# Kernel optimization log

Measured on AMD Instinct MI355X. Metric: run time of the kernel, lower is better.

The kernel has to match this reference:

```python
import math
import jax, jax.numpy as jnp
import numpy as np

B, S, C = 2048, 64, 142
D, H, DH, FF, L = 256, 8, 32, 512, 3
E, K = 128, 1024
EPS = 1e-5

def _ln(x, g, b):
    m = jnp.mean(x, -1, keepdims=True)
    v = jnp.var(x, -1, keepdims=True)
    return (x - m) * jax.lax.rsqrt(v + EPS) * g + b

def _pe(seq_len, d):
    pos = jnp.arange(seq_len, dtype=jnp.float32)[:, None]
    div = jnp.exp(jnp.arange(0, d, 2, dtype=jnp.float32) * (-math.log(10000.0) / d))
    pe = jnp.zeros((seq_len, d), jnp.float32)
    pe = pe.at[:, 0::2].set(jnp.sin(pos * div))
    pe = pe.at[:, 1::2].set(jnp.cos(pos * div))
    return pe

def setup_inputs() -> dict:
    key = jax.random.key(0)
    ks = iter(jax.random.split(key, 40))
    r = lambda shape, s=0.02: jax.random.normal(next(ks), shape, jnp.float32) * s
    inp = {
        'x': jax.random.normal(next(ks), (B, S, C), jnp.float32),
        'W_in': r((D, C)), 'b_in': jnp.zeros((D,), jnp.float32),
        'cls_token': jax.random.normal(next(ks), (1, 1, D), jnp.float32),
        'Wqkv': r((L, 3 * D, D)), 'bqkv': jnp.zeros((L, 3 * D), jnp.float32),
        'Wo': r((L, D, D)), 'bo': jnp.zeros((L, D), jnp.float32),
        'W1': r((L, FF, D)), 'b1': jnp.zeros((L, FF), jnp.float32),
        'W2': r((L, D, FF)), 'b2': jnp.zeros((L, D), jnp.float32),
        'ln1_g': jnp.ones((L, D), jnp.float32), 'ln1_b': jnp.zeros((L, D), jnp.float32),
        'ln2_g': jnp.ones((L, D), jnp.float32), 'ln2_b': jnp.zeros((L, D), jnp.float32),
        'lnf_g': jnp.ones((D,), jnp.float32), 'lnf_b': jnp.zeros((D,), jnp.float32),
        'W_out': r((E, D)), 'b_out': jnp.zeros((E,), jnp.float32),
        'codebook': jax.random.normal(next(ks), (K, E), jnp.float32),
        'Wd1': r((D, E)), 'bd1': jnp.zeros((D,), jnp.float32),
        'lnd_g': jnp.ones((D,), jnp.float32), 'lnd_b': jnp.zeros((D,), jnp.float32),
        'Wd2': r((128, D)), 'bd2': jnp.zeros((128,), jnp.float32),
        'Wd3': r((2, 128)), 'bd3': jnp.zeros((2,), jnp.float32),
    }
    return inp

def _forward(x, W_in, b_in, cls_token, Wqkv, bqkv, Wo, bo, W1, b1, W2, b2,
             ln1_g, ln1_b, ln2_g, ln2_b, lnf_g, lnf_b, W_out, b_out, codebook,
             Wd1, bd1, lnd_g, lnd_b, Wd2, bd2, Wd3, bd3):
    b = x.shape[0]
    h = x @ W_in.T + b_in                      # [B,S,D]
    h = h + _pe(S, D)[None]
    h = jnp.concatenate([jnp.broadcast_to(cls_token, (b, 1, D)), h], axis=1)  # [B,T,D]
    T = S + 1
    for i in range(L):
        qkv = h @ Wqkv[i].T + bqkv[i]          # [B,T,3D]
        q, k, v = jnp.split(qkv, 3, axis=-1)
        q = q.reshape(b, T, H, DH).transpose(0, 2, 1, 3)
        k = k.reshape(b, T, H, DH).transpose(0, 2, 1, 3)
        v = v.reshape(b, T, H, DH).transpose(0, 2, 1, 3)
        scores = jnp.einsum('bhqd,bhkd->bhqk', q, k) / math.sqrt(DH)
        attn = jax.nn.softmax(scores, axis=-1)
        o = jnp.einsum('bhqk,bhkd->bhqd', attn, v).transpose(0, 2, 1, 3).reshape(b, T, D)
        h = _ln(h + (o @ Wo[i].T + bo[i]), ln1_g[i], ln1_b[i])
        ff = jax.nn.gelu(h @ W1[i].T + b1[i], approximate=False) @ W2[i].T + b2[i]
        h = _ln(h + ff, ln2_g[i], ln2_b[i])
    cls_out = h[:, 0, :]
    z_e = _ln(cls_out, lnf_g, lnf_b) @ W_out.T + b_out   # [B,E]
    # --- EMA VQ (eval): squared-dist argmin + codebook gather ---
    d2 = (jnp.sum(z_e * z_e, -1, keepdims=True)
          - 2.0 * (z_e @ codebook.T)
          + jnp.sum(codebook * codebook, -1)[None, :])   # [B,K]
    indices = jnp.argmin(d2, axis=-1)                    # [B]
    z_q = codebook[indices]                              # gather [B,E]
    commitment_loss = 0.1 * jnp.mean((jax.lax.stop_gradient(z_q) - z_e) ** 2)
    z_q_st = z_e + jax.lax.stop_gradient(z_q - z_e)      # straight-through
    avg_probs = jnp.zeros((K,), jnp.float32).at[indices].add(1.0) / b
    perplexity = jnp.exp(-jnp.sum(avg_probs * jnp.log(avg_probs + 1e-10)))
    # --- decoder ---
    d = jax.nn.gelu(_ln(z_q_st @ Wd1.T + bd1, lnd_g, lnd_b), approximate=False)
    d = jax.nn.gelu(d @ Wd2.T + bd2, approximate=False)
    velocity_pred = d @ Wd3.T + bd3                      # [B,2]
    return velocity_pred, indices, commitment_loss, perplexity

def reference(x, W_in, b_in, cls_token, Wqkv, bqkv, Wo, bo, W1, b1, W2, b2,
              ln1_g, ln1_b, ln2_g, ln2_b, lnf_g, lnf_b, W_out, b_out, codebook,
              Wd1, bd1, lnd_g, lnd_b, Wd2, bd2, Wd3, bd3):
    return _forward(x, W_in, b_in, cls_token, Wqkv, bqkv, Wo, bo, W1, b1, W2, b2,
                    ln1_g, ln1_b, ln2_g, ln2_b, lnf_g, lnf_b, W_out, b_out, codebook,
                    Wd1, bd1, lnd_g, lnd_b, Wd2, bd2, Wd3, bd3)
```

## Files before the change

kernel.cpp:

```cpp
#include <hip/hip_runtime.h>
#include <math.h>

#define NB   2048
#define SEQ  64
#define CIN  142
#define DM   256
#define NH   8
#define DHD  32
#define FFD  512
#define NL   3
#define ED   128
#define KCB  1024
#define TT   65
#define NT   512

#define E_TOT    1572864
#define OFF_WO   589824
#define OFF_W1   786432
#define OFF_W2   1179648
#define WS_NEED  (4224 + 4 * E_TOT)

typedef __attribute__((ext_vector_type(4))) float f32x4;
typedef __attribute__((ext_vector_type(8))) _Float16 f16x8;
typedef __attribute__((ext_vector_type(4))) _Float16 f16x4;
typedef __attribute__((ext_vector_type(2))) _Float16 f16x2;

#define LO_SCALE 2048.0f
#define LO_INV   (1.0f / 2048.0f)

__device__ __forceinline__ float gelu_f(float x) {
  return 0.5f * x * (1.0f + erff(x * 0.70710678118654752f));
}

__device__ __forceinline__ float wave_bsum(float v) {
#pragma unroll
  for (int off = 32; off >= 1; off >>= 1) v += __shfl_xor(v, off, 64);
  return v;
}
__device__ __forceinline__ float wave_bmax(float v) {
#pragma unroll
  for (int off = 32; off >= 1; off >>= 1) v = fmaxf(v, __shfl_xor(v, off, 64));
  return v;
}

__device__ __forceinline__ int pidx(int pitch, int t, int c) {
  return t * pitch + ((((c >> 3) ^ (t & 7)) << 3) | (c & 7));
}

__device__ __forceinline__ void split4v(f32x4 v, f16x4& hi, f16x4& lo) {
#pragma unroll
  for (int j = 0; j < 4; ++j) {
    _Float16 h = (_Float16)v[j];
    hi[j] = h;
    lo[j] = (_Float16)((v[j] - (float)h) * LO_SCALE);
  }
}

__device__ __forceinline__ void pair_store4(_Float16* dH, _Float16* dL, int pitch,
                                            int t, int o, f32x4 v) {
  f16x4 hi, lo;
  split4v(v, hi, lo);
  int off = pidx(pitch, t, o);
  *(f16x4*)&dH[off] = hi;
  *(f16x4*)&dL[off] = lo;
}
__device__ __forceinline__ f32x4 pair_load4(const _Float16* dH, const _Float16* dL,
                                            int pitch, int t, int o) {
  int off = pidx(pitch, t, o);
  f16x4 hi = *(const f16x4*)&dH[off];
  f16x4 lo = *(const f16x4*)&dL[off];
  f32x4 v;
#pragma unroll
  for (int j = 0; j < 4; ++j) v[j] = (float)hi[j] + (float)lo[j] * LO_INV;
  return v;
}

__device__ __forceinline__ void split8_arr(const float* vv, f16x8& hi, f16x8& lo) {
#pragma unroll
  for (int j = 0; j < 8; ++j) {
    _Float16 h = (_Float16)vv[j];
    hi[j] = h;
    lo[j] = (_Float16)((vv[j] - (float)h) * LO_SCALE);
  }
}
__device__ __forceinline__ void split8_f4(const float* p, f16x8& hi, f16x8& lo) {
  float4 v0 = *(const float4*)p;
  float4 v1 = *(const float4*)(p + 4);
  float vv[8] = {v0.x, v0.y, v0.z, v0.w, v1.x, v1.y, v1.z, v1.w};
  split8_arr(vv, hi, lo);
}
__device__ __forceinline__ void split8_f2(const float* p, f16x8& hi, f16x8& lo) {
  float vv[8];
#pragma unroll
  for (int j = 0; j < 4; ++j) {
    float2 v = *(const float2*)(p + 2 * j);
    vv[2 * j] = v.x;
    vv[2 * j + 1] = v.y;
  }
  split8_arr(vv, hi, lo);
}

template <int TTN, int CIT, bool GUARDO, int WMODE>
__device__ __forceinline__ void mfma_gemm2(
    f32x4 (&acc1)[CIT][TTN], f32x4 (&acc2)[CIT][TTN],
    const float* __restrict__ Wg, const _Float16* __restrict__ WgH,
    const _Float16* __restrict__ WgL, int wld, int rbase, int rsel, int otiles,
    const _Float16* aH, const _Float16* aL, int apitch, int tRows,
    int kdim, int kvalid, int wave, int lane) {
  const int q4 = lane >> 4, cl = lane & 15;
  if (GUARDO && wave >= otiles) return;
  int wrow[CIT];
  bool oval[CIT];
#pragma unroll
  for (int ci = 0; ci < CIT; ++ci) {
    int ot = wave + 8 * ci;
    oval[ci] = !GUARDO || (ot < otiles);
    int r = ot * 16 + cl;
    int grow = rbase + (r & 31) + rsel * (r >> 5);
    wrow[ci] = grow * wld;
  }
  f16x8 zf;
#pragma unroll
  for (int j = 0; j < 8; ++j) zf[j] = (_Float16)0.f;
#pragma unroll 1
  for (int kc = 0; kc < kdim; kc += 32) {
    f16x8 bh[CIT], bl[CIT];
#pragma unroll
    for (int ci = 0; ci < CIT; ++ci) {
      if (oval[ci]) {
        if (WMODE == 2) {
          int off = wrow[ci] + kc + 8 * q4;
          bh[ci] = *(const f16x8*)&WgH[off];
          bl[ci] = *(const f16x8*)&WgL[off];
        } else if (WMODE == 1) {
          split8_f4(Wg + wrow[ci] + kc + 8 * q4, bh[ci], bl[ci]);
        } else {
          const float* wp = Wg + wrow[ci] + kc + 8 * q4;
          int cb = kc + 8 * q4;
          float vv[8];
#pragma unroll
          for (int j = 0; j < 8; ++j) vv[j] = (cb + j < kvalid) ? wp[j] : 0.f;
          split8_arr(vv, bh[ci], bl[ci]);
        }
      } else {
        bh[ci] = zf;
        bl[ci] = zf;
      }
    }
#pragma unroll
    for (int tt = 0; tt < TTN; ++tt) {
      int t = 16 * tt + cl;
      f16x8 ah, al;
      if (t < tRows) {
        int off = t * apitch + (((((kc >> 3) + q4) ^ (t & 7))) << 3);
        ah = *(const f16x8*)&aH[off];
        al = *(const f16x8*)&aL[off];
      } else {
        ah = zf;
        al = zf;
      }
#pragma unroll
      for (int ci = 0; ci < CIT; ++ci) {
        if (oval[ci]) {
          acc1[ci][tt] = __builtin_amdgcn_mfma_f32_16x16x32_f16(bh[ci], ah, acc1[ci][tt], 0, 0, 0);
          acc2[ci][tt] = __builtin_amdgcn_mfma_f32_16x16x32_f16(bh[ci], al, acc2[ci][tt], 0, 0, 0);
          acc2[ci][tt] = __builtin_amdgcn_mfma_f32_16x16x32_f16(bl[ci], ah, acc2[ci][tt], 0, 0, 0);
        }
      }
    }
  }
}

__device__ __forceinline__ void qkv_epi(const f32x4* a1, const f32x4* a2, int nt,
                                        int base, int tvalid,
                                        const float* __restrict__ bqkv_l, int hd,
                                        float* Qf, float* Kf, float* VT, float* ex,
                                        int wave, int lane) {
  if (wave >= 6) return;
  const int q4 = lane >> 4, cl = lane & 15;
  for (int tt = 0; tt < nt; ++tt) {
    int tl = 16 * tt + cl;
    if (tl < tvalid) {
      int t = base + tl;
#pragma unroll
      for (int rg = 0; rg < 4; ++rg) {
        int c = wave * 16 + q4 * 4 + rg;
        int d = c & 31;
        float v = a1[tt][rg] + a2[tt][rg] * LO_INV +
                  bqkv_l[(c >> 5) * 256 + hd * 32 + d];
        if (c < 32)      { if (t < 64) Qf[t * 36 + d] = v; else ex[d] = v; }
        else if (c < 64) { if (t < 64) Kf[t * 36 + d] = v; else ex[32 + d] = v; }
        else             VT[d * 66 + t] = v;
      }
    }
  }
}

__device__ __forceinline__ void proj_epi(const f32x4* a1, const f32x4* a2, int nt,
                                         int base, int tvalid, int half,
                                         const float* __restrict__ bo_l,
                                         _Float16* hH, _Float16* hL,
                                         int wave, int lane) {
  const int q4 = lane >> 4, cl = lane & 15;
  for (int tt = 0; tt < nt; ++tt) {
    int tl = 16 * tt + cl;
    if (tl < tvalid) {
      int t = base + tl;
      int o = half * 128 + wave * 16 + q4 * 4;
      f32x4 r = pair_load4(hH, hL, 256, t, o);
      float4 b4 = *(const float4*)&bo_l[o];
      float bb[4] = {b4.x, b4.y, b4.z, b4.w};
      f32x4 v;
#pragma unroll
      for (int rg = 0; rg < 4; ++rg)
        v[rg] = r[rg] + a1[tt][rg] + a2[tt][rg] * LO_INV + bb[rg];
      pair_store4(hH, hL, 256, t, o, v);
    }
  }
}

__device__ __forceinline__ void ln_rows_pair(_Float16* hH, _Float16* hL,
                                             const float* g, const float* be,
                                             int wave, int lane) {
  for (int t = wave; t < TT; t += 8) {
    int c0 = 2 * lane, c1 = 128 + 2 * lane;
    int o0 = pidx(256, t, c0), o1 = pidx(256, t, c1);
    f16x2 h0 = *(f16x2*)&hH[o0], l0 = *(f16x2*)&hL[o0];
    f16x2 h1 = *(f16x2*)&hH[o1], l1 = *(f16x2*)&hL[o1];
    float v0 = (float)h0[0] + (float)l0[0] * LO_INV;
    float v1 = (float)h0[1] + (float)l0[1] * LO_INV;
    float v2 = (float)h1[0] + (float)l1[0] * LO_INV;
    float v3 = (float)h1[1] + (float)l1[1] * LO_INV;
    float m = wave_bsum(v0 + v1 + v2 + v3) * (1.0f / 256.0f);
    float d0 = v0 - m, d1 = v1 - m, d2 = v2 - m, d3 = v3 - m;
    float var = wave_bsum(d0 * d0 + d1 * d1 + d2 * d2 + d3 * d3) * (1.0f / 256.0f);
    float rstd = 1.0f / sqrtf(var + 1e-5f);
    float2 g0 = *(const float2*)&g[c0], g1 = *(const float2*)&g[c1];
    float2 b0 = *(const float2*)&be[c0], b1 = *(const float2*)&be[c1];
    float r0 = d0 * rstd * g0.x + b0.x;
    float r1 = d1 * rstd * g0.y + b0.y;
    float r2 = d2 * rstd * g1.x + b1.x;
    float r3 = d3 * rstd * g1.y + b1.y;
    f16x2 nh0, nl0, nh1, nl1;
    nh0[0] = (_Float16)r0; nl0[0] = (_Float16)((r0 - (float)nh0[0]) * LO_SCALE);
    nh0[1] = (_Float16)r1; nl0[1] = (_Float16)((r1 - (float)nh0[1]) * LO_SCALE);
    nh1[0] = (_Float16)r2; nl1[0] = (_Float16)((r2 - (float)nh1[0]) * LO_SCALE);
    nh1[1] = (_Float16)r3; nl1[1] = (_Float16)((r3 - (float)nh1[1]) * LO_SCALE);
    *(f16x2*)&hH[o0] = nh0; *(f16x2*)&hL[o0] = nl0;
    *(f16x2*)&hH[o1] = nh1; *(f16x2*)&hL[o1] = nl1;
  }
}

template <int WM>
__device__ __forceinline__ void ff_pass0(const float* __restrict__ W1_l,
                                         const float* __restrict__ b1_l,
                                         const float* __restrict__ W2_l,
                                         const float* __restrict__ b2_l,
                                         const _Float16* __restrict__ W1H,
                                         const _Float16* __restrict__ W1L,
                                         const _Float16* __restrict__ W2H,
                                         const _Float16* __restrict__ W2L,
                                         _Float16* hH, _Float16* hL,
                                         _Float16* f1H, _Float16* f1L,
                                         int wave, int lane) {
  const int q4 = lane >> 4, cl = lane & 15;
  const f32x4 Z4 = {0.f, 0.f, 0.f, 0.f};
  for (int half = 0; half < 2; ++half) {
    f32x4 a1[2][2], a2[2][2];
#pragma unroll
    for (int ci = 0; ci < 2; ++ci)
#pragma unroll
      for (int tt = 0; tt < 2; ++tt) { a1[ci][tt] = Z4; a2[ci][tt] = Z4; }
    mfma_gemm2<2, 2, false, WM>(a1, a2, W1_l, W1H, W1L, DM, half * 256, 32, 16,
                                hH, hL, 256, 32, DM, DM, wave, lane);
#pragma unroll
    for (int ci = 0; ci < 2; ++ci)
#pragma unroll
      for (int tt = 0; tt < 2; ++tt) {
        int t = 16 * tt + cl;
        int m = half * 256 + (wave + 8 * ci) * 16 + q4 * 4;
        float4 b4 = *(const float4*)&b1_l[m];
        float bb[4] = {b4.x, b4.y, b4.z, b4.w};
        f32x4 v;
#pragma unroll
        for (int rg = 0; rg < 4; ++rg)
          v[rg] = gelu_f(a1[ci][tt][rg] + a2[ci][tt][rg] * LO_INV + bb[rg]);
        pair_store4(f1H, f1L, 512, t, m, v);
      }
  }
  __syncthreads();
  {
    f32x4 a1[2][2], a2[2][2];
#pragma unroll
    for (int ci = 0; ci < 2; ++ci)
#pragma unroll
      for (int tt = 0; tt < 2; ++tt) { a1[ci][tt] = Z4; a2[ci][tt] = Z4; }
    mfma_gemm2<2, 2, false, WM>(a1, a2, W2_l, W2H, W2L, FFD, 0, 32, 16,
                                f1H, f1L, 512, 32, FFD, FFD, wave, lane);
#pragma unroll
    for (int ci = 0; ci < 2; ++ci)
#pragma unroll
      for (int tt = 0; tt < 2; ++tt) {
        int t = 16 * tt + cl;
        int o = (wave + 8 * ci) * 16 + q4 * 4;
        f32x4 r = pair_load4(hH, hL, 256, t, o);
        float4 b4 = *(const float4*)&b2_l[o];
        float bb[4] = {b4.x, b4.y, b4.z, b4.w};
        f32x4 v;
#pragma unroll
        for (int rg = 0; rg < 4; ++rg)
          v[rg] = r[rg] + a1[ci][tt][rg] + a2[ci][tt][rg] * LO_INV + bb[rg];
        pair_store4(hH, hL, 256, t, o, v);
      }
  }
}

template <int WM>
__device__ __forceinline__ void ff_pass1(const float* __restrict__ W1_l,
                                         const float* __restrict__ b1_l,
                                         const float* __restrict__ W2_l,
                                         const float* __restrict__ b2_l,
                                         const _Float16* __restrict__ W1H,
                                         const _Float16* __restrict__ W1L,
                                         const _Float16* __restrict__ W2H,
                                         const _Float16* __restrict__ W2L,
                                         _Float16* hH, _Float16* hL,
                                         _Float16* f1H, _Float16* f1L,
                                         int wave, int lane) {
  const int q4 = lane >> 4, cl = lane & 15;
  const f32x4 Z4 = {0.f, 0.f, 0.f, 0.f};
  for (int cg = 0; cg < 4; ++cg) {
    f32x4 a1[1][3], a2[1][3];
#pragma unroll
    for (int tt = 0; tt < 3; ++tt) { a1[0][tt] = Z4; a2[0][tt] = Z4; }
    mfma_gemm2<3, 1, false, WM>(a1, a2, W1_l, W1H, W1L, DM, cg * 128, 32, 8,
                                hH + 32 * 256, hL + 32 * 256, 256, 33, DM, DM,
                                wave, lane);
#pragma unroll
    for (int tt = 0; tt < 3; ++tt) {
      int tl = 16 * tt + cl;
      if (tl < 33) {
        int m = cg * 128 + wave * 16 + q4 * 4;
        float4 b4 = *(const float4*)&b1_l[m];
        float bb[4] = {b4.x, b4.y, b4.z, b4.w};
        f32x4 v;
#pragma unroll
        for (int rg = 0; rg < 4; ++rg)
          v[rg] = gelu_f(a1[0][tt][rg] + a2[0][tt][rg] * LO_INV + bb[rg]);
        pair_store4(f1H, f1L, 512, tl, m, v);
      }
    }
  }
  __syncthreads();
  for (int cg = 0; cg < 2; ++cg) {
    f32x4 a1[1][3], a2[1][3];
#pragma unroll
    for (int tt = 0; tt < 3; ++tt) { a1[0][tt] = Z4; a2[0][tt] = Z4; }
    mfma_gemm2<3, 1, false, WM>(a1, a2, W2_l, W2H, W2L, FFD, cg * 128, 32, 8,
                                f1H, f1L, 512, 33, FFD, FFD, wave, lane);
#pragma unroll
    for (int tt = 0; tt < 3; ++tt) {
      int tl = 16 * tt + cl;
      if (tl < 33) {
        int t = 32 + tl;
        int o = cg * 128 + wave * 16 + q4 * 4;
        f32x4 r = pair_load4(hH, hL, 256, t, o);
        float4 b4 = *(const float4*)&b2_l[o];
        float bb[4] = {b4.x, b4.y, b4.z, b4.w};
        f32x4 v;
#pragma unroll
        for (int rg = 0; rg < 4; ++rg)
          v[rg] = r[rg] + a1[0][tt][rg] + a2[0][tt][rg] * LO_INV + bb[rg];
        pair_store4(hH, hL, 256, t, o, v);
      }
    }
  }
}

__global__ void vqvae_zero(float* __restrict__ ws) {
  int i = blockIdx.x * blockDim.x + threadIdx.x;
  if (i < 1025) ws[i] = 0.f;
}

__global__ void vqvae_prep(const float* __restrict__ Wqkv,
                           const float* __restrict__ Wo,
                           const float* __restrict__ W1,
                           const float* __restrict__ W2,
                           float* __restrict__ ws) {
  _Float16* PH = (_Float16*)(ws + 1056);
  _Float16* PL = PH + E_TOT;
  for (int i = blockIdx.x * blockDim.x + threadIdx.x; i < E_TOT;
       i += gridDim.x * blockDim.x) {
    float v;
    if (i < OFF_WO)      v = Wqkv[i];
    else if (i < OFF_W1) v = Wo[i - OFF_WO];
    else if (i < OFF_W2) v = W1[i - OFF_W1];
    else                 v = W2[i - OFF_W2];
    _Float16 h = (_Float16)v;
    PH[i] = h;
    PL[i] = (_Float16)((v - (float)h) * LO_SCALE);
  }
}

__global__ __attribute__((amdgpu_flat_work_group_size(512, 512), amdgpu_waves_per_eu(2, 2)))
void vqvae_main(
    const float* __restrict__ x, const float* __restrict__ W_in,
    const float* __restrict__ b_in, const float* __restrict__ cls_token,
    const float* __restrict__ Wqkv, const float* __restrict__ bqkv,
    const float* __restrict__ Wo, const float* __restrict__ bo,
    const float* __restrict__ W1, const float* __restrict__ b1,
    const float* __restrict__ W2, const float* __restrict__ b2,
    const float* __restrict__ ln1_g, const float* __restrict__ ln1_b,
    const float* __restrict__ ln2_g, const float* __restrict__ ln2_b,
    const float* __restrict__ lnf_g, const float* __restrict__ lnf_b,
    const float* __restrict__ W_out, const float* __restrict__ b_out,
    const float* __restrict__ codebook, const float* __restrict__ Wd1,
    const float* __restrict__ bd1, const float* __restrict__ lnd_g,
    const float* __restrict__ lnd_b, const float* __restrict__ Wd2,
    const float* __restrict__ bd2, const float* __restrict__ Wd3,
    const float* __restrict__ bd3, float* __restrict__ out,
    float* __restrict__ ws, int usePre) {
  __shared__ __align__(16) float hbuf[16640];
  __shared__ __align__(16) float obuf[16896];
  __shared__ __align__(16) float scr[6768];

  const int tid = threadIdx.x;
  const int b = blockIdx.x;
  const int lane = tid & 63, wave = tid >> 6;
  const int q4 = lane >> 4, cl = lane & 15;
  const f32x4 Z4 = {0.f, 0.f, 0.f, 0.f};
  _Float16* hH = (_Float16*)hbuf;
  _Float16* hL = hH + 65 * 256;
  const _Float16* WH = (const _Float16*)(ws + 1056);
  const _Float16* WL = WH + E_TOT;

  {
    _Float16* xH = (_Float16*)obuf;
    _Float16* xL = xH + 64 * 256;
    for (int f = tid; f < SEQ * 160; f += NT) {
      int r = f / 160, c = f - r * 160;
      float v = (c < CIN) ? x[(size_t)b * (SEQ * CIN) + r * CIN + c] : 0.f;
      _Float16 h = (_Float16)v;
      int off = pidx(256, r, c);
      xH[off] = h;
      xL[off] = (_Float16)((v - (float)h) * LO_SCALE);
    }
    if (tid < DM) {
      float v = cls_token[tid];
      _Float16 h = (_Float16)v;
      hH[tid] = h;
      hL[tid] = (_Float16)((v - (float)h) * LO_SCALE);
    }
    __syncthreads();
    for (int half = 0; half < 2; ++half) {
      for (int tg = 0; tg < 2; ++tg) {
        f32x4 a1[1][2], a2[1][2];
#pragma unroll
        for (int tt = 0; tt < 2; ++tt) { a1[0][tt] = Z4; a2[0][tt] = Z4; }
        mfma_gemm2<2, 1, false, 0>(a1, a2, W_in, nullptr, nullptr, CIN,
                                   half * 128, 32, 8, xH + 32 * tg * 256,
                                   xL + 32 * tg * 256, 256, 32, 160, CIN,
                                   wave, lane);
#pragma unroll
        for (int tt = 0; tt < 2; ++tt) {
          int t = 32 * tg + 16 * tt + cl;
          int o = half * 128 + wave * 16 + q4 * 4;
          f32x4 v;
#pragma unroll
          for (int rg = 0; rg < 4; ++rg) {
            int d = o + rg;
            float div = expf(-(float)(d & ~1) * (9.210340371976184f / 256.0f));
            float ang = (float)t * div;
            float pe = (d & 1) ? cosf(ang) : sinf(ang);
            v[rg] = a1[0][tt][rg] + a2[0][tt][rg] * LO_INV + b_in[d] + pe;
          }
          pair_store4(hH, hL, 256, t + 1, o, v);
        }
      }
    }
  }
  __syncthreads();

  for (int li = 0; li < NL; ++li) {
    const float* Wqkv_l = Wqkv + (size_t)li * 768 * DM;
    const float* bqkv_l = bqkv + li * 768;
    const float* Wo_l = Wo + (size_t)li * DM * DM;
    const float* bo_l = bo + li * DM;
    const float* W1_l = W1 + (size_t)li * FFD * DM;
    const float* b1_l = b1 + li * FFD;
    const float* W2_l = W2 + (size_t)li * DM * FFD;
    const float* b2_l = b2 + li * DM;
    const _Float16* WqkvH_l = WH + (size_t)li * 768 * DM;
    const _Float16* WqkvL_l = WL + (size_t)li * 768 * DM;
    const _Float16* WoH_l = WH + OFF_WO + (size_t)li * DM * DM;
    const _Float16* WoL_l = WL + OFF_WO + (size_t)li * DM * DM;
    const _Float16* W1H_l = WH + OFF_W1 + (size_t)li * FFD * DM;
    const _Float16* W1L_l = WL + OFF_W1 + (size_t)li * FFD * DM;
    const _Float16* W2H_l = WH + OFF_W2 + (size_t)li * DM * FFD;
    const _Float16* W2L_l = WL + OFF_W2 + (size_t)li * DM * FFD;
    _Float16* oH = (_Float16*)obuf;
    _Float16* oL = oH + 65 * 256;
    float* ex = obuf + 16640;

    for (int hd = 0; hd < NH; ++hd) {
      float* Qf = scr;
      float* Kf = scr + 2304;
      float* VT = scr + 4608;
      float* Sb = scr;
      {
        f32x4 a1[1][3], a2[1][3];
#pragma unroll
        for (int tt = 0; tt < 3; ++tt) { a1[0][tt] = Z4; a2[0][tt] = Z4; }
        if (usePre)
          mfma_gemm2<3, 1, true, 2>(a1, a2, nullptr, WqkvH_l, WqkvL_l, DM,
                                    hd * 32, 256, 6, hH, hL, 256, 48, DM, DM,
                                    wave, lane);
        else
          mfma_gemm2<3, 1, true, 1>(a1, a2, Wqkv_l, nullptr, nullptr, DM,
                                    hd * 32, 256, 6, hH, hL, 256, 48, DM, DM,
                                    wave, lane);
        __syncthreads();
        qkv_epi(&a1[0][0], &a2[0][0], 3, 0, 48, bqkv_l, hd, Qf, Kf, VT, ex,
                wave, lane);
        f32x4 c1[1][2], c2[1][2];
#pragma unroll
        for (int tt = 0; tt < 2; ++tt) { c1[0][tt] = Z4; c2[0][tt] = Z4; }
        if (usePre)
          mfma_gemm2<2, 1, true, 2>(c1, c2, nullptr, WqkvH_l, WqkvL_l, DM,
                                    hd * 32, 256, 6, hH + 48 * 256,
                                    hL + 48 * 256, 256, 17, DM, DM, wave, lane);
        else
          mfma_gemm2<2, 1, true, 1>(c1, c2, Wqkv_l, nullptr, nullptr, DM,
                                    hd * 32, 256, 6, hH + 48 * 256,
                                    hL + 48 * 256, 256, 17, DM, DM, wave, lane);
        qkv_epi(&c1[0][0], &c2[0][0], 2, 48, 17, bqkv_l, hd, Qf, Kf, VT, ex,
                wave, lane);
      }
      __syncthreads();
      f32x4 s1[4], s2[4];
      if (wave < 4) {
#pragma unroll
        for (int i = 0; i < 4; ++i) { s1[i] = Z4; s2[i] = Z4; }
        f16x8 bh, bl;
        split8_f4(&Kf[(16 * wave + cl) * 36 + 8 * q4], bh, bl);
#pragma unroll
        for (int rt = 0; rt < 4; ++rt) {
          f16x8 ah, al;
          split8_f4(&Qf[(16 * rt + cl) * 36 + 8 * q4], ah, al);
          s1[rt] = __builtin_amdgcn_mfma_f32_16x16x32_f16(ah, bh, s1[rt], 0, 0, 0);
          s2[rt] = __builtin_amdgcn_mfma_f32_16x16x32_f16(ah, bl, s2[rt], 0, 0, 0);
          s2[rt] = __builtin_amdgcn_mfma_f32_16x16x32_f16(al, bh, s2[rt], 0, 0, 0);
        }
      } else {
        const int tt4 = wave - 4;
        {
          float vv[8];
#pragma unroll
          for (int j = 0; j < 8; ++j) {
            float v = ex[32 + 8 * q4 + j];
            vv[j] = (cl == 0) ? v : 0.f;
          }
          f16x8 kh, kl;
          split8_arr(vv, kh, kl);
          f16x8 qh, ql;
          split8_f4(&Qf[(16 * tt4 + cl) * 36 + 8 * q4], qh, ql);
          f32x4 c1 = Z4, c2 = Z4;
          c1 = __builtin_amdgcn_mfma_f32_16x16x32_f16(qh, kh, c1, 0, 0, 0);
          c2 = __builtin_amdgcn_mfma_f32_16x16x32_f16(qh, kl, c2, 0, 0, 0);
          c2 = __builtin_amdgcn_mfma_f32_16x16x32_f16(ql, kh, c2, 0, 0, 0);
          if (cl == 0) {
#pragma unroll
            for (int rg = 0; rg < 4; ++rg)
              ex[64 + 16 * tt4 + q4 * 4 + rg] = c1[rg] + c2[rg] * LO_INV;
          }
        }
        {
          float vv[8];
#pragma unroll
          for (int j = 0; j < 8; ++j) {
            float v = ex[8 * q4 + j];
            vv[j] = (cl == 0) ? v : 0.f;
          }
          f16x8 qh, ql;
          split8_arr(vv, qh, ql);
          f16x8 kh, kl;
          split8_f4(&Kf[(16 * tt4 + cl) * 36 + 8 * q4], kh, kl);
          f32x4 r1 = Z4, r2 = Z4;
          r1 = __builtin_amdgcn_mfma_f32_16x16x32_f16(qh, kh, r1, 0, 0, 0);
          r2 = __builtin_amdgcn_mfma_f32_16x16x32_f16(qh, kl, r2, 0, 0, 0);
          r2 = __builtin_amdgcn_mfma_f32_16x16x32_f16(ql, kh, r2, 0, 0, 0);
          if (q4 == 0) ex[128 + 16 * tt4 + cl] = r1[0] + r2[0] * LO_INV;
        }
        if (wave == 4) {
          float p = ex[lane & 31] * ex[32 + (lane & 31)];
          p = wave_bsum(p) * 0.5f;
          if (lane == 0) ex[128 + 64] = p;
        }
      }
      __syncthreads();
      if (wave < 4) {
#pragma unroll
        for (int rt = 0; rt < 4; ++rt)
#pragma unroll
          for (int rg = 0; rg < 4; ++rg)
            Sb[(rt * 16 + q4 * 4 + rg) * 66 + wave * 16 + cl] =
                s1[rt][rg] + s2[rt][rg] * LO_INV;
      } else if (wave == 4) {
        Sb[lane * 66 + 64] = ex[64 + lane];
      } else if (wave == 5) {
        Sb[64 * 66 + lane] = ex[128 + lane];
        if (lane == 0) Sb[64 * 66 + 64] = ex[128 + 64];
      }
      __syncthreads();
      {
        const float sc = 0.17677669529663687f;
        for (int t = wave; t < 65; t += 8) {
          float s = Sb[t * 66 + lane] * sc;
          float s64 = Sb[t * 66 + 64] * sc;
          float m = fmaxf(wave_bmax(s), s64);
          float e = __expf(s - m), e64 = __expf(s64 - m);
          float inv = 1.0f / (wave_bsum(e) + e64);
          Sb[t * 66 + lane] = e * inv;
          if (lane == 0) Sb[t * 66 + 64] = e64 * inv;
        }
      }
      __syncthreads();
      {
        int rt = wave >> 1, ct = wave & 1;
        f32x4 o1 = Z4, o2 = Z4;
#pragma unroll
        for (int kc = 0; kc < 64; kc += 32) {
          f16x8 ph, pl, vh, vl;
          split8_f2(&Sb[(16 * rt + cl) * 66 + kc + 8 * q4], ph, pl);
          split8_f2(&VT[(16 * ct + cl) * 66 + kc + 8 * q4], vh, vl);
          o1 = __builtin_amdgcn_mfma_f32_16x16x32_f16(vh, ph, o1, 0, 0, 0);
          o2 = __builtin_amdgcn_mfma_f32_16x16x32_f16(vh, pl, o2, 0, 0, 0);
          o2 = __builtin_amdgcn_mfma_f32_16x16x32_f16(vl, ph, o2, 0, 0, 0);
        }
        int t = rt * 16 + cl;
        float p64 = Sb[t * 66 + 64];
        int ob = ct * 16 + q4 * 4;
        f32x4 v;
#pragma unroll
        for (int rg = 0; rg < 4; ++rg) {
          int d = ob + rg;
          v[rg] = o1[rg] + o2[rg] * LO_INV + p64 * VT[d * 66 + 64];
        }
        pair_store4(oH, oL, 256, t, hd * 32 + ob, v);
      }
      if (wave == 0) {
        int d = lane & 31, hf = lane >> 5;
        float o = 0.f;
        for (int u = hf * 32; u < hf * 32 + 32; ++u)
          o += Sb[64 * 66 + u] * VT[d * 66 + u];
        if (hf == 1) o += Sb[64 * 66 + 64] * VT[d * 66 + 64];
        o += __shfl_down(o, 32, 64);
        if (lane < 32) {
          int c = hd * 32 + d;
          _Float16 h = (_Float16)o;
          int off = pidx(256, 64, c);
          oH[off] = h;
          oL[off] = (_Float16)((o - (float)h) * LO_SCALE);
        }
      }
    }
    __syncthreads();

    for (int half = 0; half < 2; ++half) {
      {
        f32x4 a1[1][3], a2[1][3];
#pragma unroll
        for (int tt = 0; tt < 3; ++tt) { a1[0][tt] = Z4; a2[0][tt] = Z4; }
        if (usePre)
          mfma_gemm2<3, 1, false, 2>(a1, a2, nullptr, WoH_l, WoL_l, DM,
                                     half * 128, 32, 8, oH, oL, 256, 48, DM,
                                     DM, wave, lane);
        else
          mfma_gemm2<3, 1, false, 1>(a1, a2, Wo_l, nullptr, nullptr, DM,
                                     half * 128, 32, 8, oH, oL, 256, 48, DM,
                                     DM, wave, lane);
        proj_epi(&a1[0][0], &a2[0][0], 3, 0, 48, half, bo_l, hH, hL, wave, lane);
      }
      {
        f32x4 a1[1][2], a2[1][2];
#pragma unroll
        for (int tt = 0; tt < 2; ++tt) { a1[0][tt] = Z4; a2[0][tt] = Z4; }
        if (usePre)
          mfma_gemm2<2, 1, false, 2>(a1, a2, nullptr, WoH_l, WoL_l, DM,
                                     half * 128, 32, 8, oH + 48 * 256,
                                     oL + 48 * 256, 256, 17, DM, DM, wave, lane);
        else
          mfma_gemm2<2, 1, false, 1>(a1, a2, Wo_l, nullptr, nullptr, DM,
                                     half * 128, 32, 8, oH + 48 * 256,
                                     oL + 48 * 256, 256, 17, DM, DM, wave, lane);
        proj_epi(&a1[0][0], &a2[0][0], 2, 48, 17, half, bo_l, hH, hL, wave, lane);
      }
    }
    __syncthreads();
    ln_rows_pair(hH, hL, ln1_g + li * DM, ln1_b + li * DM, wave, lane);
    __syncthreads();

    {
      _Float16* f1H = (_Float16*)obuf;
      _Float16* f1L = f1H + 33 * 512;
      if (usePre) {
        ff_pass0<2>(W1_l, b1_l, W2_l, b2_l, W1H_l, W1L_l, W2H_l, W2L_l,
                    hH, hL, f1H, f1L, wave, lane);
        __syncthreads();
        ff_pass1<2>(W1_l, b1_l, W2_l, b2_l, W1H_l, W1L_l, W2H_l, W2L_l,
                    hH, hL, f1H, f1L, wave, lane);
      } else {
        ff_pass0<1>(W1_l, b1_l, W2_l, b2_l, nullptr, nullptr, nullptr, nullptr,
                    hH, hL, f1H, f1L, wave, lane);
        __syncthreads();
        ff_pass1<1>(W1_l, b1_l, W2_l, b2_l, nullptr, nullptr, nullptr, nullptr,
                    hH, hL, f1H, f1L, wave, lane);
      }
    }
    __syncthreads();
    ln_rows_pair(hH, hL, ln2_g + li * DM, ln2_b + li * DM, wave, lane);
    __syncthreads();
  }

  if (tid < 64) {
    int c0 = 2 * lane, c1 = 128 + 2 * lane;
    float v0 = (float)hH[c0] + (float)hL[c0] * LO_INV;
    float v1 = (float)hH[c0 + 1] + (float)hL[c0 + 1] * LO_INV;
    float v2 = (float)hH[c1] + (float)hL[c1] * LO_INV;
    float v3 = (float)hH[c1 + 1] + (float)hL[c1 + 1] * LO_INV;
    float m = wave_bsum(v0 + v1 + v2 + v3) * (1.0f / 256.0f);
    float d0 = v0 - m, d1 = v1 - m, d2 = v2 - m, d3 = v3 - m;
    float var = wave_bsum(d0 * d0 + d1 * d1 + d2 * d2 + d3 * d3) * (1.0f / 256.0f);
    float rstd = 1.0f / sqrtf(var + 1e-5f);
    obuf[c0]     = d0 * rstd * lnf_g[c0]     + lnf_b[c0];
    obuf[c0 + 1] = d1 * rstd * lnf_g[c0 + 1] + lnf_b[c0 + 1];
    obuf[c1]     = d2 * rstd * lnf_g[c1]     + lnf_b[c1];
    obuf[c1 + 1] = d3 * rstd * lnf_g[c1 + 1] + lnf_b[c1 + 1];
  }
  __syncthreads();
  for (int o = wave; o < ED; o += 8) {
    const float4 w4 = *(const float4*)&W_out[o * DM + lane * 4];
    const float4 c4 = *(const float4*)&obuf[lane * 4];
    float s = w4.x * c4.x + w4.y * c4.y + w4.z * c4.z + w4.w * c4.w;
    s = wave_bsum(s);
    if (lane == 0) obuf[256 + o] = s + b_out[o];
  }
  __syncthreads();

  float bestv = 3.4e38f;
  int bestk = 0;
  for (int ch = 0; ch < 8; ++ch) {
    __syncthreads();
    for (int f = tid; f < 128 * 128; f += NT) {
      int r = f >> 7, c = f & 127;
      hbuf[r * 129 + c] = codebook[(size_t)(ch * 128 + r) * ED + c];
    }
    __syncthreads();
    {
      int kl = tid & 127, q = tid >> 7;
      float part = 0.f;
#pragma unroll 8
      for (int jj = 0; jj < 32; ++jj) {
        int e = q * 32 + jj;
        float cv = hbuf[kl * 129 + e];
        part += cv * (cv - 2.0f * obuf[256 + e]);
      }
      scr[kl * 4 + q] = part;
    }
    __syncthreads();
    if (tid < 128) {
      float d2v = scr[tid * 4] + scr[tid * 4 + 1] + scr[tid * 4 + 2] + scr[tid * 4 + 3];
      int kk = ch * 128 + tid;
      if (d2v < bestv) { bestv = d2v; bestk = kk; }
    }
  }
  if (tid < 128) {
    scr[512 + tid] = bestv;
    scr[640 + tid] = __int_as_float(bestk);
  }
  __syncthreads();
  if (tid == 0) {
    float bv = 3.4e38f;
    int bk = 1 << 30;
    for (int j = 0; j < 128; ++j) {
      float v = scr[512 + j];
      int kk = __float_as_int(scr[640 + j]);
      if (v < bv || (v == bv && kk < bk)) { bv = v; bk = kk; }
    }
    scr[700] = __int_as_float(bk);
    out[2 * NB + b] = (float)bk;
  }
  __syncthreads();
  const int bk = __float_as_int(scr[700]);

  if (tid < ED) {
    float zqv = codebook[(size_t)bk * ED + tid];
    obuf[384 + tid] = zqv;
    float df = zqv - obuf[256 + tid];
    float sq = wave_bsum(df * df);
    if ((tid & 63) == 0) atomicAdd(&ws[0], sq);
  }
  if (tid == 0) atomicAdd(&ws[1 + bk], 1.0f);
  __syncthreads();

  for (int o = wave; o < DM; o += 8) {
    const float2 w2 = *(const float2*)&Wd1[o * ED + lane * 2];
    const float2 z2 = *(const float2*)&obuf[384 + lane * 2];
    float s = wave_bsum(w2.x * z2.x + w2.y * z2.y);
    if (lane == 0) obuf[512 + o] = s + bd1[o];
  }
  __syncthreads();
  if (tid < 64) {
    float v0 = obuf[512 + lane], v1 = obuf[512 + lane + 64];
    float v2 = obuf[512 + lane + 128], v3 = obuf[512 + lane + 192];
    float m = wave_bsum(v0 + v1 + v2 + v3) * (1.0f / 256.0f);
    float d0 = v0 - m, d1 = v1 - m, d2 = v2 - m, d3 = v3 - m;
    float var = wave_bsum(d0 * d0 + d1 * d1 + d2 * d2 + d3 * d3) * (1.0f / 256.0f);
    float rstd = 1.0f / sqrtf(var + 1e-5f);
    obuf[512 + lane]       = gelu_f(d0 * rstd * lnd_g[lane]       + lnd_b[lane]);
    obuf[512 + lane + 64]  = gelu_f(d1 * rstd * lnd_g[lane + 64]  + lnd_b[lane + 64]);
    obuf[512 + lane + 128] = gelu_f(d2 * rstd * lnd_g[lane + 128] + lnd_b[lane + 128]);
    obuf[512 + lane + 192] = gelu_f(d3 * rstd * lnd_g[lane + 192] + lnd_b[lane + 192]);
  }
  __syncthreads();
  for (int o = wave; o < ED; o += 8) {
    const float4 w4 = *(const float4*)&Wd2[o * DM + lane * 4];
    const float4 g4 = *(const float4*)&obuf[512 + lane * 4];
    float s = wave_bsum(w4.x * g4.x + w4.y * g4.y + w4.z * g4.z + w4.w * g4.w);
    if (lane == 0) obuf[768 + o] = gelu_f(s + bd2[o]);
  }
  __syncthreads();
  if (wave < 2) {
    const float2 w2 = *(const float2*)&Wd3[wave * ED + lane * 2];
    const float2 g2 = *(const float2*)&obuf[768 + lane * 2];
    float s = wave_bsum(w2.x * g2.x + w2.y * g2.y);
    if (lane == 0) out[b * 2 + wave] = s + bd3[wave];
  }
}

__global__ void vqvae_finish(const float* __restrict__ ws, float* __restrict__ out) {
  __shared__ float red[256];
  int tid = threadIdx.x;
  float part = 0.f;
  for (int k = tid; k < KCB; k += 256) {
    float p = ws[1 + k] * (1.0f / 2048.0f);
    part += p * logf(p + 1e-10f);
  }
  red[tid] = part;
  __syncthreads();
  for (int s = 128; s > 0; s >>= 1) {
    if (tid < s) red[tid] += red[tid + s];
    __syncthreads();
  }
  if (tid == 0) {
    out[2 * NB + NB]     = 0.1f * ws[0] * (1.0f / (2048.0f * 128.0f));
    out[2 * NB + NB + 1] = expf(-red[0]);
  }
}

extern "C" void kernel_launch(void* const* d_in, const int* in_sizes, int n_in,
                              void* d_out, int out_size, void* d_ws, size_t ws_size,
                              hipStream_t stream) {
  (void)in_sizes; (void)n_in; (void)out_size;
  const float* x         = (const float*)d_in[0];
  const float* W_in      = (const float*)d_in[1];
  const float* b_in      = (const float*)d_in[2];
  const float* cls_token = (const float*)d_in[3];
  const float* Wqkv      = (const float*)d_in[4];
  const float* bqkv      = (const float*)d_in[5];
  const float* Wo        = (const float*)d_in[6];
  const float* bo        = (const float*)d_in[7];
  const float* W1        = (const float*)d_in[8];
  const float* b1        = (const float*)d_in[9];
  const float* W2        = (const float*)d_in[10];
  const float* b2        = (const float*)d_in[11];
  const float* ln1_g     = (const float*)d_in[12];
  const float* ln1_b     = (const float*)d_in[13];
  const float* ln2_g     = (const float*)d_in[14];
  const float* ln2_b     = (const float*)d_in[15];
  const float* lnf_g     = (const float*)d_in[16];
  const float* lnf_b     = (const float*)d_in[17];
  const float* W_out     = (const float*)d_in[18];
  const float* b_out     = (const float*)d_in[19];
  const float* codebook  = (const float*)d_in[20];
  const float* Wd1       = (const float*)d_in[21];
  const float* bd1       = (const float*)d_in[22];
  const float* lnd_g     = (const float*)d_in[23];
  const float* lnd_b     = (const float*)d_in[24];
  const float* Wd2       = (const float*)d_in[25];
  const float* bd2       = (const float*)d_in[26];
  const float* Wd3       = (const float*)d_in[27];
  const float* bd3       = (const float*)d_in[28];
  float* out = (float*)d_out;
  float* ws = (float*)d_ws;

  const int usePre = (ws_size >= (size_t)WS_NEED) ? 1 : 0;

  hipLaunchKernelGGL(vqvae_zero, dim3(5), dim3(256), 0, stream, ws);
  if (usePre)
    hipLaunchKernelGGL(vqvae_prep, dim3(2048), dim3(512), 0, stream,
                       Wqkv, Wo, W1, W2, ws);
  hipLaunchKernelGGL(vqvae_main, dim3(NB), dim3(NT), 0, stream,
                     x, W_in, b_in, cls_token, Wqkv, bqkv, Wo, bo, W1, b1, W2, b2,
                     ln1_g, ln1_b, ln2_g, ln2_b, lnf_g, lnf_b, W_out, b_out,
                     codebook, Wd1, bd1, lnd_g, lnd_b, Wd2, bd2, Wd3, bd3, out,
                     ws, usePre);
  hipLaunchKernelGGL(vqvae_finish, dim3(1), dim3(256), 0, stream, ws, out);
}
```

Measured before the change: 5.816 ms.

## Double block to 16 waves and repartition all GEMM and attention work

Measured after the change: 6.585 ms. 1.13x slower.

```diff
diff --git a/kernel.cpp b/kernel.cpp
--- a/kernel.cpp
+++ b/kernel.cpp
@@ -12,7 +12,8 @@
 #define ED   128
 #define KCB  1024
 #define TT   65
-#define NT   512
+#define NT   1024
+#define NW   16
 
 #define E_TOT    1572864
 #define OFF_WO   589824
@@ -100,24 +101,21 @@
   split8_arr(vv, hi, lo);
 }
 
-template <int TTN, int CIT, bool GUARDO, int WMODE>
-__device__ __forceinline__ void mfma_gemm2(
+template <int TTN, int CIT, int WMODE>
+__device__ __forceinline__ void mfma_gw(
     f32x4 (&acc1)[CIT][TTN], f32x4 (&acc2)[CIT][TTN],
     const float* __restrict__ Wg, const _Float16* __restrict__ WgH,
-    const _Float16* __restrict__ WgL, int wld, int rbase, int rsel, int otiles,
+    const _Float16* __restrict__ WgL, int wld, int rbase, int rsel,
+    int ot0, int otstride,
     const _Float16* aH, const _Float16* aL, int apitch, int tRows,
-    int kdim, int kvalid, int wave, int lane) {
+    int kdim, int kvalid, int lane) {
+  if (ot0 < 0) return;
   const int q4 = lane >> 4, cl = lane & 15;
-  if (GUARDO && wave >= otiles) return;
   int wrow[CIT];
-  bool oval[CIT];
 #pragma unroll
   for (int ci = 0; ci < CIT; ++ci) {
-    int ot = wave + 8 * ci;
-    oval[ci] = !GUARDO || (ot < otiles);
-    int r = ot * 16 + cl;
-    int grow = rbase + (r & 31) + rsel * (r >> 5);
-    wrow[ci] = grow * wld;
+    int r = (ot0 + otstride * ci) * 16 + cl;
+    wrow[ci] = (rbase + (r & 31) + rsel * (r >> 5)) * wld;
   }
   f16x8 zf;
 #pragma unroll
@@ -127,24 +125,19 @@
     f16x8 bh[CIT], bl[CIT];
 #pragma unroll
     for (int ci = 0; ci < CIT; ++ci) {
-      if (oval[ci]) {
-        if (WMODE == 2) {
-          int off = wrow[ci] + kc + 8 * q4;
-          bh[ci] = *(const f16x8*)&WgH[off];
-          bl[ci] = *(const f16x8*)&WgL[off];
-        } else if (WMODE == 1) {
-          split8_f4(Wg + wrow[ci] + kc + 8 * q4, bh[ci], bl[ci]);
-        } else {
-          const float* wp = Wg + wrow[ci] + kc + 8 * q4;
-          int cb = kc + 8 * q4;
-          float vv[8];
-#pragma unroll
-          for (int j = 0; j < 8; ++j) vv[j] = (cb + j < kvalid) ? wp[j] : 0.f;
-          split8_arr(vv, bh[ci], bl[ci]);
-        }
+      if (WMODE == 2) {
+        int off = wrow[ci] + kc + 8 * q4;
+        bh[ci] = *(const f16x8*)&WgH[off];
+        bl[ci] = *(const f16x8*)&WgL[off];
+      } else if (WMODE == 1) {
+        split8_f4(Wg + wrow[ci] + kc + 8 * q4, bh[ci], bl[ci]);
       } else {
-        bh[ci] = zf;
-        bl[ci] = zf;
+        const float* wp = Wg + wrow[ci] + kc + 8 * q4;
+        int cb = kc + 8 * q4;
+        float vv[8];
+#pragma unroll
+        for (int j = 0; j < 8; ++j) vv[j] = (cb + j < kvalid) ? wp[j] : 0.f;
+        split8_arr(vv, bh[ci], bl[ci]);
       }
     }
 #pragma unroll
@@ -161,22 +154,19 @@
       }
 #pragma unroll
       for (int ci = 0; ci < CIT; ++ci) {
-        if (oval[ci]) {
-          acc1[ci][tt] = __builtin_amdgcn_mfma_f32_16x16x32_f16(bh[ci], ah, acc1[ci][tt], 0, 0, 0);
-          acc2[ci][tt] = __builtin_amdgcn_mfma_f32_16x16x32_f16(bh[ci], al, acc2[ci][tt], 0, 0, 0);
-          acc2[ci][tt] = __builtin_amdgcn_mfma_f32_16x16x32_f16(bl[ci], ah, acc2[ci][tt], 0, 0, 0);
-        }
-      }
-    }
-  }
-}
-
-__device__ __forceinline__ void qkv_epi(const f32x4* a1, const f32x4* a2, int nt,
-                                        int base, int tvalid,
-                                        const float* __restrict__ bqkv_l, int hd,
-                                        float* Qf, float* Kf, float* VT, float* ex,
-                                        int wave, int lane) {
-  if (wave >= 6) return;
+        acc1[ci][tt] = __builtin_amdgcn_mfma_f32_16x16x32_f16(bh[ci], ah, acc1[ci][tt], 0, 0, 0);
+        acc2[ci][tt] = __builtin_amdgcn_mfma_f32_16x16x32_f16(bh[ci], al, acc2[ci][tt], 0, 0, 0);
+        acc2[ci][tt] = __builtin_amdgcn_mfma_f32_16x16x32_f16(bl[ci], ah, acc2[ci][tt], 0, 0, 0);
+      }
+    }
+  }
+}
+
+__device__ __forceinline__ void qkv_epi2(const f32x4* a1, const f32x4* a2,
+                                         int nt, int base, int tvalid, int ot,
+                                         const float* __restrict__ bqkv_l, int hd,
+                                         float* Qf, float* Kf, float* VT,
+                                         float* ex, int lane) {
   const int q4 = lane >> 4, cl = lane & 15;
   for (int tt = 0; tt < nt; ++tt) {
     int tl = 16 * tt + cl;
@@ -184,7 +174,7 @@
       int t = base + tl;
 #pragma unroll
       for (int rg = 0; rg < 4; ++rg) {
-        int c = wave * 16 + q4 * 4 + rg;
+        int c = ot * 16 + q4 * 4 + rg;
         int d = c & 31;
         float v = a1[tt][rg] + a2[tt][rg] * LO_INV +
                   bqkv_l[(c >> 5) * 256 + hd * 32 + d];
@@ -196,17 +186,16 @@
   }
 }
 
-__device__ __forceinline__ void proj_epi(const f32x4* a1, const f32x4* a2, int nt,
-                                         int base, int tvalid, int half,
-                                         const float* __restrict__ bo_l,
-                                         _Float16* hH, _Float16* hL,
-                                         int wave, int lane) {
+__device__ __forceinline__ void proj_epi2(const f32x4* a1, const f32x4* a2,
+                                          int nt, int base, int tvalid, int ot,
+                                          const float* __restrict__ bo_l,
+                                          _Float16* hH, _Float16* hL, int lane) {
   const int q4 = lane >> 4, cl = lane & 15;
   for (int tt = 0; tt < nt; ++tt) {
     int tl = 16 * tt + cl;
     if (tl < tvalid) {
       int t = base + tl;
-      int o = half * 128 + wave * 16 + q4 * 4;
+      int o = ot * 16 + q4 * 4;
       f32x4 r = pair_load4(hH, hL, 256, t, o);
       float4 b4 = *(const float4*)&bo_l[o];
       float bb[4] = {b4.x, b4.y, b4.z, b4.w};
@@ -219,10 +208,221 @@
   }
 }
 
+template <int WM>
+__device__ __forceinline__ void qkv_phase(
+    const float* __restrict__ Wq, const _Float16* __restrict__ WqH,
+    const _Float16* __restrict__ WqL, const float* __restrict__ bqkv_l, int hd,
+    const _Float16* hH, const _Float16* hL,
+    float* Qf, float* Kf, float* VT, float* ex, int wave, int lane) {
+  const f32x4 Z4 = {0.f, 0.f, 0.f, 0.f};
+  f32x4 b1a[1][2], b2a[1][2], s1a[1][1], s2a[1][1], s1b[1][1], s2b[1][1];
+#pragma unroll
+  for (int tt = 0; tt < 2; ++tt) { b1a[0][tt] = Z4; b2a[0][tt] = Z4; }
+  s1a[0][0] = Z4; s2a[0][0] = Z4; s1b[0][0] = Z4; s2b[0][0] = Z4;
+  const int bigot = (wave < 12) ? (wave >> 1) : -1;
+  const int bigbase = (wave & 1) * 32;
+  const int sot1 = (wave >= 12) ? (wave - 12) : -1;
+  const int sot2 = (wave == 12) ? 4 : ((wave == 13) ? 5 : -1);
+  mfma_gw<2, 1, WM>(b1a, b2a, Wq, WqH, WqL, DM, hd * 32, 256, bigot, 16,
+                    hH + bigbase * 256, hL + bigbase * 256, 256, 32, DM, DM,
+                    lane);
+  mfma_gw<1, 1, WM>(s1a, s2a, Wq, WqH, WqL, DM, hd * 32, 256, sot1, 16,
+                    hH + 64 * 256, hL + 64 * 256, 256, 1, DM, DM, lane);
+  mfma_gw<1, 1, WM>(s1b, s2b, Wq, WqH, WqL, DM, hd * 32, 256, sot2, 16,
+                    hH + 64 * 256, hL + 64 * 256, 256, 1, DM, DM, lane);
+  __syncthreads();
+  if (bigot >= 0)
+    qkv_epi2(&b1a[0][0], &b2a[0][0], 2, bigbase, 32, bigot, bqkv_l, hd,
+             Qf, Kf, VT, ex, lane);
+  if (sot1 >= 0)
+    qkv_epi2(&s1a[0][0], &s2a[0][0], 1, 64, 1, sot1, bqkv_l, hd,
+             Qf, Kf, VT, ex, lane);
+  if (sot2 >= 0)
+    qkv_epi2(&s1b[0][0], &s2b[0][0], 1, 64, 1, sot2, bqkv_l, hd,
+             Qf, Kf, VT, ex, lane);
+}
+
+template <int WM>
+__device__ __forceinline__ void proj_phase(
+    const float* __restrict__ Wo_l, const _Float16* __restrict__ WoH,
+    const _Float16* __restrict__ WoL, const float* __restrict__ bo_l,
+    const _Float16* oH, const _Float16* oL,
+    _Float16* hH, _Float16* hL, int wave, int lane) {
+  const f32x4 Z4 = {0.f, 0.f, 0.f, 0.f};
+  {
+    f32x4 a1[1][2], a2[1][2];
+#pragma unroll
+    for (int tt = 0; tt < 2; ++tt) { a1[0][tt] = Z4; a2[0][tt] = Z4; }
+    mfma_gw<2, 1, WM>(a1, a2, Wo_l, WoH, WoL, DM, 0, 32, wave, 16,
+                      oH, oL, 256, 32, DM, DM, lane);
+    proj_epi2(&a1[0][0], &a2[0][0], 2, 0, 32, wave, bo_l, hH, hL, lane);
+  }
+  {
+    f32x4 a1[1][2], a2[1][2];
+#pragma unroll
+    for (int tt = 0; tt < 2; ++tt) { a1[0][tt] = Z4; a2[0][tt] = Z4; }
+    mfma_gw<2, 1, WM>(a1, a2, Wo_l, WoH, WoL, DM, 0, 32, wave, 16,
+                      oH + 32 * 256, oL + 32 * 256, 256, 32, DM, DM, lane);
+    proj_epi2(&a1[0][0], &a2[0][0], 2, 32, 32, wave, bo_l, hH, hL, lane);
+  }
+  {
+    f32x4 a1[1][1], a2[1][1];
+    a1[0][0] = Z4; a2[0][0] = Z4;
+    mfma_gw<1, 1, WM>(a1, a2, Wo_l, WoH, WoL, DM, 0, 32, wave, 16,
+                      oH + 64 * 256, oL + 64 * 256, 256, 1, DM, DM, lane);
+    proj_epi2(&a1[0][0], &a2[0][0], 1, 64, 1, wave, bo_l, hH, hL, lane);
+  }
+}
+
+template <int WM>
+__device__ __forceinline__ void ff_pass0(
+    const float* __restrict__ W1_l, const float* __restrict__ b1_l,
+    const float* __restrict__ W2_l, const float* __restrict__ b2_l,
+    const _Float16* __restrict__ W1H, const _Float16* __restrict__ W1L,
+    const _Float16* __restrict__ W2H, const _Float16* __restrict__ W2L,
+    _Float16* hH, _Float16* hL, _Float16* f1H, _Float16* f1L,
+    int wave, int lane) {
+  const int q4 = lane >> 4, cl = lane & 15;
+  const f32x4 Z4 = {0.f, 0.f, 0.f, 0.f};
+  {
+    f32x4 a1[2][2], a2[2][2];
+#pragma unroll
+    for (int ci = 0; ci < 2; ++ci)
+#pragma unroll
+      for (int tt = 0; tt < 2; ++tt) { a1[ci][tt] = Z4; a2[ci][tt] = Z4; }
+    mfma_gw<2, 2, WM>(a1, a2, W1_l, W1H, W1L, DM, 0, 32, wave, 16,
+                      hH, hL, 256, 32, DM, DM, lane);
+#pragma unroll
+    for (int ci = 0; ci < 2; ++ci)
+#pragma unroll
+      for (int tt = 0; tt < 2; ++tt) {
+        int t = 16 * tt + cl;
+        int m = (wave + 16 * ci) * 16 + q4 * 4;
+        float4 b4 = *(const float4*)&b1_l[m];
+        float bb[4] = {b4.x, b4.y, b4.z, b4.w};
+        f32x4 v;
+#pragma unroll
+        for (int rg = 0; rg < 4; ++rg)
+          v[rg] = gelu_f(a1[ci][tt][rg] + a2[ci][tt][rg] * LO_INV + bb[rg]);
+        pair_store4(f1H, f1L, 512, t, m, v);
+      }
+  }
+  __syncthreads();
+  {
+    f32x4 a1[1][2], a2[1][2];
+#pragma unroll
+    for (int tt = 0; tt < 2; ++tt) { a1[0][tt] = Z4; a2[0][tt] = Z4; }
+    mfma_gw<2, 1, WM>(a1, a2, W2_l, W2H, W2L, FFD, 0, 32, wave, 16,
+                      f1H, f1L, 512, 32, FFD, FFD, lane);
+#pragma unroll
+    for (int tt = 0; tt < 2; ++tt) {
+      int t = 16 * tt + cl;
+      int o = wave * 16 + q4 * 4;
+      f32x4 r = pair_load4(hH, hL, 256, t, o);
+      float4 b4 = *(const float4*)&b2_l[o];
+      float bb[4] = {b4.x, b4.y, b4.z, b4.w};
+      f32x4 v;
+#pragma unroll
+      for (int rg = 0; rg < 4; ++rg)
+        v[rg] = r[rg] + a1[0][tt][rg] + a2[0][tt][rg] * LO_INV + bb[rg];
+      pair_store4(hH, hL, 256, t, o, v);
+    }
+  }
+}
+
+template <int WM>
+__device__ __forceinline__ void ff_pass1(
+    const float* __restrict__ W1_l, const float* __restrict__ b1_l,
+    const float* __restrict__ W2_l, const float* __restrict__ b2_l,
+    const _Float16* __restrict__ W1H, const _Float16* __restrict__ W1L,
+    const _Float16* __restrict__ W2H, const _Float16* __restrict__ W2L,
+    _Float16* hH, _Float16* hL, _Float16* f1H, _Float16* f1L,
+    int wave, int lane) {
+  const int q4 = lane >> 4, cl = lane & 15;
+  const f32x4 Z4 = {0.f, 0.f, 0.f, 0.f};
+  {
+    f32x4 a1[2][2], a2[2][2];
+#pragma unroll
+    for (int ci = 0; ci < 2; ++ci)
+#pragma unroll
+      for (int tt = 0; tt < 2; ++tt) { a1[ci][tt] = Z4; a2[ci][tt] = Z4; }
+    mfma_gw<2, 2, WM>(a1, a2, W1_l, W1H, W1L, DM, 0, 32, wave, 16,
+                      hH + 32 * 256, hL + 32 * 256, 256, 32, DM, DM, lane);
+#pragma unroll
+    for (int ci = 0; ci < 2; ++ci)
+#pragma unroll
+      for (int tt = 0; tt < 2; ++tt) {
+        int tl = 16 * tt + cl;
+        int m = (wave + 16 * ci) * 16 + q4 * 4;
+        float4 b4 = *(const float4*)&b1_l[m];
+        float bb[4] = {b4.x, b4.y, b4.z, b4.w};
+        f32x4 v;
+#pragma unroll
+        for (int rg = 0; rg < 4; ++rg)
+          v[rg] = gelu_f(a1[ci][tt][rg] + a2[ci][tt][rg] * LO_INV + bb[rg]);
+        pair_store4(f1H, f1L, 512, tl, m, v);
+      }
+    f32x4 c1[2][1], c2[2][1];
+#pragma unroll
+    for (int ci = 0; ci < 2; ++ci) { c1[ci][0] = Z4; c2[ci][0] = Z4; }
+    mfma_gw<1, 2, WM>(c1, c2, W1_l, W1H, W1L, DM, 0, 32, wave, 16,
+                      hH + 64 * 256, hL + 64 * 256, 256, 1, DM, DM, lane);
+#pragma unroll
+    for (int ci = 0; ci < 2; ++ci) {
+      if (cl < 1) {
+        int m = (wave + 16 * ci) * 16 + q4 * 4;
+        float4 b4 = *(const float4*)&b1_l[m];
+        float bb[4] = {b4.x, b4.y, b4.z, b4.w};
+        f32x4 v;
+#pragma unroll
+        for (int rg = 0; rg < 4; ++rg)
+          v[rg] = gelu_f(c1[ci][0][rg] + c2[ci][0][rg] * LO_INV + bb[rg]);
+        pair_store4(f1H, f1L, 512, 32, m, v);
+      }
+    }
+  }
+  __syncthreads();
+  {
+    f32x4 a1[1][2], a2[1][2];
+#pragma unroll
+    for (int tt = 0; tt < 2; ++tt) { a1[0][tt] = Z4; a2[0][tt] = Z4; }
+    mfma_gw<2, 1, WM>(a1, a2, W2_l, W2H, W2L, FFD, 0, 32, wave, 16,
+                      f1H, f1L, 512, 32, FFD, FFD, lane);
+#pragma unroll
+    for (int tt = 0; tt < 2; ++tt) {
+      int t = 32 + 16 * tt + cl;
+      int o = wave * 16 + q4 * 4;
+      f32x4 r = pair_load4(hH, hL, 256, t, o);
+      float4 b4 = *(const float4*)&b2_l[o];
+      float bb[4] = {b4.x, b4.y, b4.z, b4.w};
+      f32x4 v;
+#pragma unroll
+      for (int rg = 0; rg < 4; ++rg)
+        v[rg] = r[rg] + a1[0][tt][rg] + a2[0][tt][rg] * LO_INV + bb[rg];
+      pair_store4(hH, hL, 256, t, o, v);
+    }
+    f32x4 c1[1][1], c2[1][1];
+    c1[0][0] = Z4; c2[0][0] = Z4;
+    mfma_gw<1, 1, WM>(c1, c2, W2_l, W2H, W2L, FFD, 0, 32, wave, 16,
+                      f1H + 32 * 512, f1L + 32 * 512, 512, 1, FFD, FFD, lane);
+    if (cl < 1) {
+      int o = wave * 16 + q4 * 4;
+      f32x4 r = pair_load4(hH, hL, 256, 64, o);
+      float4 b4 = *(const float4*)&b2_l[o];
+      float bb[4] = {b4.x, b4.y, b4.z, b4.w};
+      f32x4 v;
+#pragma unroll
+      for (int rg = 0; rg < 4; ++rg)
+        v[rg] = r[rg] + c1[0][0][rg] + c2[0][0][rg] * LO_INV + bb[rg];
+      pair_store4(hH, hL, 256, 64, o, v);
+    }
+  }
+}
+
 __device__ __forceinline__ void ln_rows_pair(_Float16* hH, _Float16* hL,
                                              const float* g, const float* be,
                                              int wave, int lane) {
-  for (int t = wave; t < TT; t += 8) {
+  for (int t = wave; t < TT; t += NW) {
     int c0 = 2 * lane, c1 = 128 + 2 * lane;
     int o0 = pidx(256, t, c0), o1 = pidx(256, t, c1);
     f16x2 h0 = *(f16x2*)&hH[o0], l0 = *(f16x2*)&hL[o0];
@@ -251,132 +451,6 @@
   }
 }
 
-template <int WM>
-__device__ __forceinline__ void ff_pass0(const float* __restrict__ W1_l,
-                                         const float* __restrict__ b1_l,
-                                         const float* __restrict__ W2_l,
-                                         const float* __restrict__ b2_l,
-                                         const _Float16* __restrict__ W1H,
-                                         const _Float16* __restrict__ W1L,
-                                         const _Float16* __restrict__ W2H,
-                                         const _Float16* __restrict__ W2L,
-                                         _Float16* hH, _Float16* hL,
-                                         _Float16* f1H, _Float16* f1L,
-                                         int wave, int lane) {
-  const int q4 = lane >> 4, cl = lane & 15;
-  const f32x4 Z4 = {0.f, 0.f, 0.f, 0.f};
-  for (int half = 0; half < 2; ++half) {
-    f32x4 a1[2][2], a2[2][2];
-#pragma unroll
-    for (int ci = 0; ci < 2; ++ci)
-#pragma unroll
-      for (int tt = 0; tt < 2; ++tt) { a1[ci][tt] = Z4; a2[ci][tt] = Z4; }
-    mfma_gemm2<2, 2, false, WM>(a1, a2, W1_l, W1H, W1L, DM, half * 256, 32, 16,
-                                hH, hL, 256, 32, DM, DM, wave, lane);
-#pragma unroll
-    for (int ci = 0; ci < 2; ++ci)
-#pragma unroll
-      for (int tt = 0; tt < 2; ++tt) {
-        int t = 16 * tt + cl;
-        int m = half * 256 + (wave + 8 * ci) * 16 + q4 * 4;
-        float4 b4 = *(const float4*)&b1_l[m];
-        float bb[4] = {b4.x, b4.y, b4.z, b4.w};
-        f32x4 v;
-#pragma unroll
-        for (int rg = 0; rg < 4; ++rg)
-          v[rg] = gelu_f(a1[ci][tt][rg] + a2[ci][tt][rg] * LO_INV + bb[rg]);
-        pair_store4(f1H, f1L, 512, t, m, v);
-      }
-  }
-  __syncthreads();
-  {
-    f32x4 a1[2][2], a2[2][2];
-#pragma unroll
-    for (int ci = 0; ci < 2; ++ci)
-#pragma unroll
-      for (int tt = 0; tt < 2; ++tt) { a1[ci][tt] = Z4; a2[ci][tt] = Z4; }
-    mfma_gemm2<2, 2, false, WM>(a1, a2, W2_l, W2H, W2L, FFD, 0, 32, 16,
-                                f1H, f1L, 512, 32, FFD, FFD, wave, lane);
-#pragma unroll
-    for (int ci = 0; ci < 2; ++ci)
-#pragma unroll
-      for (int tt = 0; tt < 2; ++tt) {
-        int t = 16 * tt + cl;
-        int o = (wave + 8 * ci) * 16 + q4 * 4;
-        f32x4 r = pair_load4(hH, hL, 256, t, o);
-        float4 b4 = *(const float4*)&b2_l[o];
-        float bb[4] = {b4.x, b4.y, b4.z, b4.w};
-        f32x4 v;
-#pragma unroll
-        for (int rg = 0; rg < 4; ++rg)
-          v[rg] = r[rg] + a1[ci][tt][rg] + a2[ci][tt][rg] * LO_INV + bb[rg];
-        pair_store4(hH, hL, 256, t, o, v);
-      }
-  }
-}
-
-template <int WM>
-__device__ __forceinline__ void ff_pass1(const float* __restrict__ W1_l,
-                                         const float* __restrict__ b1_l,
-                                         const float* __restrict__ W2_l,
-                                         const float* __restrict__ b2_l,
-                                         const _Float16* __restrict__ W1H,
-                                         const _Float16* __restrict__ W1L,
-                                         const _Float16* __restrict__ W2H,
-                                         const _Float16* __restrict__ W2L,
-                                         _Float16* hH, _Float16* hL,
-                                         _Float16* f1H, _Float16* f1L,
-                                         int wave, int lane) {
-  const int q4 = lane >> 4, cl = lane & 15;
-  const f32x4 Z4 = {0.f, 0.f, 0.f, 0.f};
-  for (int cg = 0; cg < 4; ++cg) {
-    f32x4 a1[1][3], a2[1][3];
-#pragma unroll
-    for (int tt = 0; tt < 3; ++tt) { a1[0][tt] = Z4; a2[0][tt] = Z4; }
-    mfma_gemm2<3, 1, false, WM>(a1, a2, W1_l, W1H, W1L, DM, cg * 128, 32, 8,
-                                hH + 32 * 256, hL + 32 * 256, 256, 33, DM, DM,
-                                wave, lane);
-#pragma unroll
-    for (int tt = 0; tt < 3; ++tt) {
-      int tl = 16 * tt + cl;
-      if (tl < 33) {
-        int m = cg * 128 + wave * 16 + q4 * 4;
-        float4 b4 = *(const float4*)&b1_l[m];
-        float bb[4] = {b4.x, b4.y, b4.z, b4.w};
-        f32x4 v;
-#pragma unroll
-        for (int rg = 0; rg < 4; ++rg)
-          v[rg] = gelu_f(a1[0][tt][rg] + a2[0][tt][rg] * LO_INV + bb[rg]);
-        pair_store4(f1H, f1L, 512, tl, m, v);
-      }
-    }
-  }
-  __syncthreads();
-  for (int cg = 0; cg < 2; ++cg) {
-    f32x4 a1[1][3], a2[1][3];
-#pragma unroll
-    for (int tt = 0; tt < 3; ++tt) { a1[0][tt] = Z4; a2[0][tt] = Z4; }
-    mfma_gemm2<3, 1, false, WM>(a1, a2, W2_l, W2H, W2L, FFD, cg * 128, 32, 8,
-                                f1H, f1L, 512, 33, FFD, FFD, wave, lane);
-#pragma unroll
-    for (int tt = 0; tt < 3; ++tt) {
-      int tl = 16 * tt + cl;
-      if (tl < 33) {
-        int t = 32 + tl;
-        int o = cg * 128 + wave * 16 + q4 * 4;
-        f32x4 r = pair_load4(hH, hL, 256, t, o);
-        float4 b4 = *(const float4*)&b2_l[o];
-        float bb[4] = {b4.x, b4.y, b4.z, b4.w};
-        f32x4 v;
-#pragma unroll
-        for (int rg = 0; rg < 4; ++rg)
-          v[rg] = r[rg] + a1[0][tt][rg] + a2[0][tt][rg] * LO_INV + bb[rg];
-        pair_store4(hH, hL, 256, t, o, v);
-      }
-    }
-  }
-}
-
 __global__ void vqvae_zero(float* __restrict__ ws) {
   int i = blockIdx.x * blockDim.x + threadIdx.x;
   if (i < 1025) ws[i] = 0.f;
@@ -402,7 +476,7 @@
   }
 }
 
-__global__ __attribute__((amdgpu_flat_work_group_size(512, 512), amdgpu_waves_per_eu(2, 2)))
+__global__ __attribute__((amdgpu_flat_work_group_size(1024, 1024), amdgpu_waves_per_eu(4, 4)))
 void vqvae_main(
     const float* __restrict__ x, const float* __restrict__ W_in,
     const float* __restrict__ b_in, const float* __restrict__ cls_token,
@@ -452,30 +526,27 @@
       hL[tid] = (_Float16)((v - (float)h) * LO_SCALE);
     }
     __syncthreads();
-    for (int half = 0; half < 2; ++half) {
-      for (int tg = 0; tg < 2; ++tg) {
-        f32x4 a1[1][2], a2[1][2];
-#pragma unroll
-        for (int tt = 0; tt < 2; ++tt) { a1[0][tt] = Z4; a2[0][tt] = Z4; }
-        mfma_gemm2<2, 1, false, 0>(a1, a2, W_in, nullptr, nullptr, CIN,
-                                   half * 128, 32, 8, xH + 32 * tg * 256,
-                                   xL + 32 * tg * 256, 256, 32, 160, CIN,
-                                   wave, lane);
-#pragma unroll
-        for (int tt = 0; tt < 2; ++tt) {
-          int t = 32 * tg + 16 * tt + cl;
-          int o = half * 128 + wave * 16 + q4 * 4;
-          f32x4 v;
-#pragma unroll
-          for (int rg = 0; rg < 4; ++rg) {
-            int d = o + rg;
-            float div = expf(-(float)(d & ~1) * (9.210340371976184f / 256.0f));
-            float ang = (float)t * div;
-            float pe = (d & 1) ? cosf(ang) : sinf(ang);
-            v[rg] = a1[0][tt][rg] + a2[0][tt][rg] * LO_INV + b_in[d] + pe;
-          }
-          pair_store4(hH, hL, 256, t + 1, o, v);
+    for (int rg = 0; rg < 2; ++rg) {
+      f32x4 a1[1][2], a2[1][2];
+#pragma unroll
+      for (int tt = 0; tt < 2; ++tt) { a1[0][tt] = Z4; a2[0][tt] = Z4; }
+      mfma_gw<2, 1, 0>(a1, a2, W_in, nullptr, nullptr, CIN, 0, 32, wave, 16,
+                       xH + rg * 32 * 256, xL + rg * 32 * 256, 256, 32, 160,
+                       CIN, lane);
+#pragma unroll
+      for (int tt = 0; tt < 2; ++tt) {
+        int t = rg * 32 + 16 * tt + cl;
+        int o = wave * 16 + q4 * 4;
+        f32x4 v;
+#pragma unroll
+        for (int rgx = 0; rgx < 4; ++rgx) {
+          int d = o + rgx;
+          float div = expf(-(float)(d & ~1) * (9.210340371976184f / 256.0f));
+          float ang = (float)t * div;
+          float pe = (d & 1) ? cosf(ang) : sinf(ang);
+          v[rgx] = a1[0][tt][rgx] + a2[0][tt][rgx] * LO_INV + b_in[d] + pe;
         }
+        pair_store4(hH, hL, 256, t + 1, o, v);
       }
     }
   }
@@ -507,105 +578,75 @@
       float* Kf = scr + 2304;
       float* VT = scr + 4608;
       float* Sb = scr;
+      if (usePre)
+        qkv_phase<2>(nullptr, WqkvH_l, WqkvL_l, bqkv_l, hd, hH, hL,
+                     Qf, Kf, VT, ex, wave, lane);
+      else
+        qkv_phase<1>(Wqkv_l, nullptr, nullptr, bqkv_l, hd, hH, hL,
+                     Qf, Kf, VT, ex, wave, lane);
+      __syncthreads();
+      f32x4 sm1 = Z4, sm2 = Z4;
       {
-        f32x4 a1[1][3], a2[1][3];
-#pragma unroll
-        for (int tt = 0; tt < 3; ++tt) { a1[0][tt] = Z4; a2[0][tt] = Z4; }
-        if (usePre)
-          mfma_gemm2<3, 1, true, 2>(a1, a2, nullptr, WqkvH_l, WqkvL_l, DM,
-                                    hd * 32, 256, 6, hH, hL, 256, 48, DM, DM,
-                                    wave, lane);
-        else
-          mfma_gemm2<3, 1, true, 1>(a1, a2, Wqkv_l, nullptr, nullptr, DM,
-                                    hd * 32, 256, 6, hH, hL, 256, 48, DM, DM,
-                                    wave, lane);
-        __syncthreads();
-        qkv_epi(&a1[0][0], &a2[0][0], 3, 0, 48, bqkv_l, hd, Qf, Kf, VT, ex,
-                wave, lane);
-        f32x4 c1[1][2], c2[1][2];
-#pragma unroll
-        for (int tt = 0; tt < 2; ++tt) { c1[0][tt] = Z4; c2[0][tt] = Z4; }
-        if (usePre)
-          mfma_gemm2<2, 1, true, 2>(c1, c2, nullptr, WqkvH_l, WqkvL_l, DM,
-                                    hd * 32, 256, 6, hH + 48 * 256,
-                                    hL + 48 * 256, 256, 17, DM, DM, wave, lane);
-        else
-          mfma_gemm2<2, 1, true, 1>(c1, c2, Wqkv_l, nullptr, nullptr, DM,
-                                    hd * 32, 256, 6, hH + 48 * 256,
-                                    hL + 48 * 256, 256, 17, DM, DM, wave, lane);
-        qkv_epi(&c1[0][0], &c2[0][0], 2, 48, 17, bqkv_l, hd, Qf, Kf, VT, ex,
-                wave, lane);
+        int rt = wave >> 2, ct = wave & 3;
+        f16x8 bh, bl, ah, al;
+        split8_f4(&Kf[(16 * ct + cl) * 36 + 8 * q4], bh, bl);
+        split8_f4(&Qf[(16 * rt + cl) * 36 + 8 * q4], ah, al);
+        sm1 = __builtin_amdgcn_mfma_f32_16x16x32_f16(ah, bh, sm1, 0, 0, 0);
+        sm2 = __builtin_amdgcn_mfma_f32_16x16x32_f16(ah, bl, sm2, 0, 0, 0);
+        sm2 = __builtin_amdgcn_mfma_f32_16x16x32_f16(al, bh, sm2, 0, 0, 0);
+      }
+      if (wave < 4) {
+        int tt4 = wave;
+        float vv[8];
+#pragma unroll
+        for (int j = 0; j < 8; ++j) {
+          float v = ex[32 + 8 * q4 + j];
+          vv[j] = (cl == 0) ? v : 0.f;
+        }
+        f16x8 kh, kl;
+        split8_arr(vv, kh, kl);
+        f16x8 qh, ql;
+        split8_f4(&Qf[(16 * tt4 + cl) * 36 + 8 * q4], qh, ql);
+        f32x4 c1 = Z4, c2 = Z4;
+        c1 = __builtin_amdgcn_mfma_f32_16x16x32_f16(qh, kh, c1, 0, 0, 0);
+        c2 = __builtin_amdgcn_mfma_f32_16x16x32_f16(qh, kl, c2, 0, 0, 0);
+        c2 = __builtin_amdgcn_mfma_f32_16x16x32_f16(ql, kh, c2, 0, 0, 0);
+        if (cl == 0) {
+#pragma unroll
+          for (int rg = 0; rg < 4; ++rg)
+            ex[64 + 16 * tt4 + q4 * 4 + rg] = c1[rg] + c2[rg] * LO_INV;
+        }
+      } else if (wave < 8) {
+        int tt4 = wave - 4;
+        float vv[8];
+#pragma unroll
+        for (int j = 0; j < 8; ++j) {
+          float v = ex[8 * q4 + j];
+          vv[j] = (cl == 0) ? v : 0.f;
+        }
+        f16x8 qh, ql;
+        split8_arr(vv, qh, ql);
+        f16x8 kh, kl;
+        split8_f4(&Kf[(16 * tt4 + cl) * 36 + 8 * q4], kh, kl);
+        f32x4 r1 = Z4, r2 = Z4;
+        r1 = __builtin_amdgcn_mfma_f32_16x16x32_f16(qh, kh, r1, 0, 0, 0);
+        r2 = __builtin_amdgcn_mfma_f32_16x16x32_f16(qh, kl, r2, 0, 0, 0);
+        r2 = __builtin_amdgcn_mfma_f32_16x16x32_f16(ql, kh, r2, 0, 0, 0);
+        if (q4 == 0) ex[128 + 16 * tt4 + cl] = r1[0] + r2[0] * LO_INV;
+      } else if (wave == 8) {
+        float p = ex[lane & 31] * ex[32 + (lane & 31)];
+        p = wave_bsum(p) * 0.5f;
+        if (lane == 0) ex[128 + 64] = p;
       }
       __syncthreads();
-      f32x4 s1[4], s2[4];
-      if (wave < 4) {
-#pragma unroll
-        for (int i = 0; i < 4; ++i) { s1[i] = Z4; s2[i] = Z4; }
-        f16x8 bh, bl;
-        split8_f4(&Kf[(16 * wave + cl) * 36 + 8 * q4], bh, bl);
-#pragma unroll
-        for (int rt = 0; rt < 4; ++rt) {
-          f16x8 ah, al;
-          split8_f4(&Qf[(16 * rt + cl) * 36 + 8 * q4], ah, al);
-          s1[rt] = __builtin_amdgcn_mfma_f32_16x16x32_f16(ah, bh, s1[rt], 0, 0, 0);
-          s2[rt] = __builtin_amdgcn_mfma_f32_16x16x32_f16(ah, bl, s2[rt], 0, 0, 0);
-          s2[rt] = __builtin_amdgcn_mfma_f32_16x16x32_f16(al, bh, s2[rt], 0, 0, 0);
-        }
-      } else {
-        const int tt4 = wave - 4;
-        {
-          float vv[8];
-#pragma unroll
-          for (int j = 0; j < 8; ++j) {
-            float v = ex[32 + 8 * q4 + j];
-            vv[j] = (cl == 0) ? v : 0.f;
-          }
-          f16x8 kh, kl;
-          split8_arr(vv, kh, kl);
-          f16x8 qh, ql;
-          split8_f4(&Qf[(16 * tt4 + cl) * 36 + 8 * q4], qh, ql);
-          f32x4 c1 = Z4, c2 = Z4;
-          c1 = __builtin_amdgcn_mfma_f32_16x16x32_f16(qh, kh, c1, 0, 0, 0);
-          c2 = __builtin_amdgcn_mfma_f32_16x16x32_f16(qh, kl, c2, 0, 0, 0);
-          c2 = __builtin_amdgcn_mfma_f32_16x16x32_f16(ql, kh, c2, 0, 0, 0);
-          if (cl == 0) {
-#pragma unroll
-            for (int rg = 0; rg < 4; ++rg)
-              ex[64 + 16 * tt4 + q4 * 4 + rg] = c1[rg] + c2[rg] * LO_INV;
-          }
-        }
-        {
-          float vv[8];
-#pragma unroll
-          for (int j = 0; j < 8; ++j) {
-            float v = ex[8 * q4 + j];
-            vv[j] = (cl == 0) ? v : 0.f;
-          }
-          f16x8 qh, ql;
-          split8_arr(vv, qh, ql);
-          f16x8 kh, kl;
-          split8_f4(&Kf[(16 * tt4 + cl) * 36 + 8 * q4], kh, kl);
-          f32x4 r1 = Z4, r2 = Z4;
-          r1 = __builtin_amdgcn_mfma_f32_16x16x32_f16(qh, kh, r1, 0, 0, 0);
-          r2 = __builtin_amdgcn_mfma_f32_16x16x32_f16(qh, kl, r2, 0, 0, 0);
-          r2 = __builtin_amdgcn_mfma_f32_16x16x32_f16(ql, kh, r2, 0, 0, 0);
-          if (q4 == 0) ex[128 + 16 * tt4 + cl] = r1[0] + r2[0] * LO_INV;
-        }
-        if (wave == 4) {
-          float p = ex[lane & 31] * ex[32 + (lane & 31)];
-          p = wave_bsum(p) * 0.5f;
-          if (lane == 0) ex[128 + 64] = p;
-        }
-      }
-      __syncthreads();
-      if (wave < 4) {
-#pragma unroll
-        for (int rt = 0; rt < 4; ++rt)
-#pragma unroll
-          for (int rg = 0; rg < 4; ++rg)
-            Sb[(rt * 16 + q4 * 4 + rg) * 66 + wave * 16 + cl] =
-                s1[rt][rg] + s2[rt][rg] * LO_INV;
-      } else if (wave == 4) {
+      {
+        int rt = wave >> 2, ct = wave & 3;
+#pragma unroll
+        for (int rg = 0; rg < 4; ++rg)
+          Sb[(rt * 16 + q4 * 4 + rg) * 66 + ct * 16 + cl] =
+              sm1[rg] + sm2[rg] * LO_INV;
+      }
+      if (wave == 4) {
         Sb[lane * 66 + 64] = ex[64 + lane];
       } else if (wave == 5) {
         Sb[64 * 66 + lane] = ex[128 + lane];
@@ -614,7 +655,7 @@
       __syncthreads();
       {
         const float sc = 0.17677669529663687f;
-        for (int t = wave; t < 65; t += 8) {
+        for (int t = wave; t < 65; t += NW) {
           float s = Sb[t * 66 + lane] * sc;
           float s64 = Sb[t * 66 + 64] * sc;
           float m = fmaxf(wave_bmax(s), s64);
@@ -625,7 +666,7 @@
         }
       }
       __syncthreads();
-      {
+      if (wave < 8) {
         int rt = wave >> 1, ct = wave & 1;
         f32x4 o1 = Z4, o2 = Z4;
 #pragma unroll
@@ -647,55 +688,28 @@
           v[rg] = o1[rg] + o2[rg] * LO_INV + p64 * VT[d * 66 + 64];
         }
         pair_store4(oH, oL, 256, t, hd * 32 + ob, v);
-      }
-      if (wave == 0) {
-        int d = lane & 31, hf = lane >> 5;
+      } else {
+        int d = (wave - 8) * 4 + q4;
         float o = 0.f;
-        for (int u = hf * 32; u < hf * 32 + 32; ++u)
-          o += Sb[64 * 66 + u] * VT[d * 66 + u];
-        if (hf == 1) o += Sb[64 * 66 + 64] * VT[d * 66 + 64];
-        o += __shfl_down(o, 32, 64);
-        if (lane < 32) {
+        for (int uu = cl; uu < 65; uu += 16)
+          o += Sb[64 * 66 + uu] * VT[d * 66 + uu];
+#pragma unroll
+        for (int off = 8; off >= 1; off >>= 1) o += __shfl_xor(o, off, 64);
+        if (cl == 0) {
           int c = hd * 32 + d;
           _Float16 h = (_Float16)o;
-          int off = pidx(256, 64, c);
-          oH[off] = h;
-          oL[off] = (_Float16)((o - (float)h) * LO_SCALE);
+          int off2 = pidx(256, 64, c);
+          oH[off2] = h;
+          oL[off2] = (_Float16)((o - (float)h) * LO_SCALE);
         }
       }
     }
     __syncthreads();
 
-    for (int half = 0; half < 2; ++half) {
-      {
-        f32x4 a1[1][3], a2[1][3];
-#pragma unroll
-        for (int tt = 0; tt < 3; ++tt) { a1[0][tt] = Z4; a2[0][tt] = Z4; }
-        if (usePre)
-          mfma_gemm2<3, 1, false, 2>(a1, a2, nullptr, WoH_l, WoL_l, DM,
-                                     half * 128, 32, 8, oH, oL, 256, 48, DM,
-                                     DM, wave, lane);
-        else
-          mfma_gemm2<3, 1, false, 1>(a1, a2, Wo_l, nullptr, nullptr, DM,
-                                     half * 128, 32, 8, oH, oL, 256, 48, DM,
-                                     DM, wave, lane);
-        proj_epi(&a1[0][0], &a2[0][0], 3, 0, 48, half, bo_l, hH, hL, wave, lane);
-      }
-      {
-        f32x4 a1[1][2], a2[1][2];
-#pragma unroll
-        for (int tt = 0; tt < 2; ++tt) { a1[0][tt] = Z4; a2[0][tt] = Z4; }
-        if (usePre)
-          mfma_gemm2<2, 1, false, 2>(a1, a2, nullptr, WoH_l, WoL_l, DM,
-                                     half * 128, 32, 8, oH + 48 * 256,
-                                     oL + 48 * 256, 256, 17, DM, DM, wave, lane);
-        else
-          mfma_gemm2<2, 1, false, 1>(a1, a2, Wo_l, nullptr, nullptr, DM,
-                                     half * 128, 32, 8, oH + 48 * 256,
-                                     oL + 48 * 256, 256, 17, DM, DM, wave, lane);
-        proj_epi(&a1[0][0], &a2[0][0], 2, 48, 17, half, bo_l, hH, hL, wave, lane);
-      }
-    }
+    if (usePre)
+      proj_phase<2>(nullptr, WoH_l, WoL_l, bo_l, oH, oL, hH, hL, wave, lane);
+    else
+      proj_phase<1>(Wo_l, nullptr, nullptr, bo_l, oH, oL, hH, hL, wave, lane);
     __syncthreads();
     ln_rows_pair(hH, hL, ln1_g + li * DM, ln1_b + li * DM, wave, lane);
     __syncthreads();
@@ -738,7 +752,7 @@
     obuf[c1 + 1] = d3 * rstd * lnf_g[c1 + 1] + lnf_b[c1 + 1];
   }
   __syncthreads();
-  for (int o = wave; o < ED; o += 8) {
+  for (int o = wave; o < ED; o += NW) {
     const float4 w4 = *(const float4*)&W_out[o * DM + lane * 4];
     const float4 c4 = *(const float4*)&obuf[lane * 4];
     float s = w4.x * c4.x + w4.y * c4.y + w4.z * c4.z + w4.w * c4.w;
@@ -759,39 +773,41 @@
     {
       int kl = tid & 127, q = tid >> 7;
       float part = 0.f;
-#pragma unroll 8
-      for (int jj = 0; jj < 32; ++jj) {
-        int e = q * 32 + jj;
+#pragma unroll 4
+      for (int jj = 0; jj < 16; ++jj) {
+        int e = q * 16 + jj;
         float cv = hbuf[kl * 129 + e];
         part += cv * (cv - 2.0f * obuf[256 + e]);
       }
-      scr[kl * 4 + q] = part;
+      scr[kl * 8 + q] = part;
     }
     __syncthreads();
     if (tid < 128) {
-      float d2v = scr[tid * 4] + scr[tid * 4 + 1] + scr[tid * 4 + 2] + scr[tid * 4 + 3];
+      float d2v = 0.f;
+#pragma unroll
+      for (int j = 0; j < 8; ++j) d2v += scr[tid * 8 + j];
       int kk = ch * 128 + tid;
       if (d2v < bestv) { bestv = d2v; bestk = kk; }
     }
   }
   if (tid < 128) {
-    scr[512 + tid] = bestv;
-    scr[640 + tid] = __int_as_float(bestk);
+    scr[1024 + tid] = bestv;
+    scr[1152 + tid] = __int_as_float(bestk);
   }
   __syncthreads();
   if (tid == 0) {
     float bv = 3.4e38f;
     int bk = 1 << 30;
     for (int j = 0; j < 128; ++j) {
-      float v = scr[512 + j];
-      int kk = __float_as_int(scr[640 + j]);
+      float v = scr[1024 + j];
+      int kk = __float_as_int(scr[1152 + j]);
       if (v < bv || (v == bv && kk < bk)) { bv = v; bk = kk; }
     }
-    scr[700] = __int_as_float(bk);
+    scr[1300] = __int_as_float(bk);
     out[2 * NB + b] = (float)bk;
   }
   __syncthreads();
-  const int bk = __float_as_int(scr[700]);
+  const int bk = __float_as_int(scr[1300]);
 
   if (tid < ED) {
     float zqv = codebook[(size_t)bk * ED + tid];
@@ -803,7 +819,7 @@
   if (tid == 0) atomicAdd(&ws[1 + bk], 1.0f);
   __syncthreads();
 
-  for (int o = wave; o < DM; o += 8) {
+  for (int o = wave; o < DM; o += NW) {
     const float2 w2 = *(const float2*)&Wd1[o * ED + lane * 2];
     const float2 z2 = *(const float2*)&obuf[384 + lane * 2];
     float s = wave_bsum(w2.x * z2.x + w2.y * z2.y);
@@ -823,7 +839,7 @@
     obuf[512 + lane + 192] = gelu_f(d3 * rstd * lnd_g[lane + 192] + lnd_b[lane + 192]);
   }
   __syncthreads();
-  for (int o = wave; o < ED; o += 8) {
+  for (int o = wave; o < ED; o += NW) {
     const float4 w4 = *(const float4*)&Wd2[o * DM + lane * 4];
     const float4 g4 = *(const float4*)&obuf[512 + lane * 4];
     float s = wave_bsum(w4.x * g4.x + w4.y * g4.y + w4.z * g4.z + w4.w * g4.w);
```
